# Optimization experiments

Hardware: AMD Instinct MI355X
Metric: run time of the kernel (lower is better)

The kernel has to match this reference:

```python
import jax, jax.numpy as jnp
import numpy as np

IN_CAPS, OUT_CAPS, OUT_DIM = 32, 10, 16


def squash(s):
    # s: [B, out_caps, out_dim]
    sq = jnp.sum(s * s, axis=2)              # [B, out_caps]
    mod = jnp.sqrt(sq)
    scale = sq / (1.0 + sq) / mod            # matches torch: sqrmod/(1+sqrmod)/mod
    return scale[..., None] * s


def setup_inputs() -> dict:
    key = jax.random.key(0)
    k1, k2 = jax.random.split(key)
    B, in_dim = 4096, 288
    caps_output = jax.random.normal(k1, (B, IN_CAPS, in_dim), dtype=jnp.float32)
    # W initialized uniform(-1/32, 1/32) in the original; scale randn similarly small
    W = jax.random.uniform(k2, (IN_CAPS, in_dim, OUT_CAPS * OUT_DIM),
                           dtype=jnp.float32, minval=-1.0 / 32, maxval=1.0 / 32)
    b = jnp.zeros((IN_CAPS, OUT_CAPS), dtype=jnp.float32)
    return {"caps_output": caps_output, "W": W, "b": b}


def reference(caps_output, W, b):
    B = caps_output.shape[0]
    # caps_output.unsqueeze(2).matmul(W): per-input-capsule matmul
    u = jnp.einsum('bni,nio->bno', caps_output, W)          # [B, 32, 160]
    u = u.reshape(B, IN_CAPS, OUT_CAPS, OUT_DIM)            # [B, 32, 10, 16]

    c = jax.nn.softmax(b, axis=1)                           # [32, 10]
    s = jnp.einsum('no,bnod->bod', c, u)                    # [B, 10, 16]
    v = squash(s)

    b_batch = jnp.broadcast_to(b, (B, IN_CAPS, OUT_CAPS))
    for _ in range(3):
        # agreement: <u_predict, v>
        b_batch = b_batch + jnp.einsum('bnod,bod->bno', u, v)
        c = jax.nn.softmax(b_batch, axis=-1)                # [B, 32, 10]
        s = jnp.einsum('bno,bnod->bod', c, u)
        v = squash(s)
    return v
```

## Files before the change

kernel.cpp:

```cpp
#include <hip/hip_runtime.h>
#include <hip/hip_bf16.h>

#define IN_CAPS 32
#define OUT_CAPS 10
#define NOUT 160
#define KDIM 288
#define BATCH 4096
#define KSTEPS 9
#define CTILES 10
#define STR2 162

typedef __bf16 bf16x8 __attribute__((ext_vector_type(8)));
typedef float  f32x4  __attribute__((ext_vector_type(4)));
typedef __attribute__((address_space(1))) void as1_t;
typedef __attribute__((address_space(3))) void as3_t;

__global__ __launch_bounds__(256) void prep_w(const float* __restrict__ W,
                                              __bf16* __restrict__ Wf) {
    int f = blockIdx.x * 256 + threadIdx.x;
    int j    = f & 7;
    int l    = (f >> 3) & 63;
    int rest = f >> 9;
    int c    = rest % CTILES;
    int tnk  = rest / CTILES;
    int ks   = tnk % KSTEPS;
    int n    = tnk / KSTEPS;
    int k    = ks * 32 + (l >> 4) * 8 + j;
    int col  = c * 16 + (l & 15);
    Wf[f] = (__bf16)W[(n * KDIM + k) * NOUT + col];
}

__global__ __launch_bounds__(256) void gemm_u(const float* __restrict__ caps,
                                              const __bf16* __restrict__ Wf,
                                              uint4* __restrict__ up) {
    __shared__ float  As[2][64 * 32];
    __shared__ __bf16 Bs[2][5120];

    const int n    = blockIdx.y;
    const int rb   = blockIdx.x;
    const int w    = threadIdx.x >> 6;
    const int lane = threadIdx.x & 63;
    const int lm   = lane & 15;
    const int lk   = lane >> 4;

    const int sl0 = w * 128 + lane;
    const int sl1 = sl0 + 64;
    const int r0 = sl0 >> 3, r1 = sl1 >> 3;
    const int c0 = (sl0 & 7) ^ (r0 & 7);
    const int c1 = (sl1 & 7) ^ (r1 & 7);
    const float* ga0 = caps + ((size_t)(rb * 64 + r0) * IN_CAPS + n) * KDIM + c0 * 4;
    const float* ga1 = caps + ((size_t)(rb * 64 + r1) * IN_CAPS + n) * KDIM + c1 * 4;

    const __bf16* wb = Wf + (size_t)n * (KSTEPS * 5120);

#define STAGE(ks, buf) do {                                                          \
    __builtin_amdgcn_global_load_lds((const as1_t*)(ga0 + (ks) * 32),                \
                                     (as3_t*)&As[buf][w * 512],        16, 0, 0);    \
    __builtin_amdgcn_global_load_lds((const as1_t*)(ga1 + (ks) * 32),                \
                                     (as3_t*)&As[buf][w * 512 + 256],  16, 0, 0);    \
    __builtin_amdgcn_global_load_lds((const as1_t*)(wb + (size_t)(ks) * 5120 +       \
                                     (w * 2) * 512 + lane * 8),                      \
                                     (as3_t*)&Bs[buf][(w * 2) * 512],  16, 0, 0);    \
    __builtin_amdgcn_global_load_lds((const as1_t*)(wb + (size_t)(ks) * 5120 +       \
                                     (w * 2 + 1) * 512 + lane * 8),                  \
                                     (as3_t*)&Bs[buf][(w * 2 + 1) * 512], 16, 0, 0); \
    if (w < 2)                                                                       \
        __builtin_amdgcn_global_load_lds((const as1_t*)(wb + (size_t)(ks) * 5120 +   \
                                         (8 + w) * 512 + lane * 8),                  \
                                         (as3_t*)&Bs[buf][(8 + w) * 512], 16, 0, 0); \
} while (0)

    f32x4 acc[CTILES];
#pragma unroll
    for (int ct = 0; ct < CTILES; ++ct) acc[ct] = (f32x4){0.f, 0.f, 0.f, 0.f};

    const int rl = w * 16 + lm;
    const int h0 = ((2 * lk)     ^ (lm & 7)) * 4;
    const int h1 = ((2 * lk + 1) ^ (lm & 7)) * 4;

    STAGE(0, 0);
    __syncthreads();

    for (int ks = 0; ks < KSTEPS; ++ks) {
        if (ks + 1 < KSTEPS) STAGE(ks + 1, (ks + 1) & 1);

        const float*  Ac = As[ks & 1];
        const __bf16* Bc = Bs[ks & 1];
        f32x4 x0 = *(const f32x4*)&Ac[rl * 32 + h0];
        f32x4 x1 = *(const f32x4*)&Ac[rl * 32 + h1];
        bf16x8 a;
        a[0] = (__bf16)x0[0]; a[1] = (__bf16)x0[1];
        a[2] = (__bf16)x0[2]; a[3] = (__bf16)x0[3];
        a[4] = (__bf16)x1[0]; a[5] = (__bf16)x1[1];
        a[6] = (__bf16)x1[2]; a[7] = (__bf16)x1[3];

#pragma unroll
        for (int ct = 0; ct < CTILES; ++ct) {
            bf16x8 bfr = *(const bf16x8*)&Bc[ct * 512 + lane * 8];
            acc[ct] = __builtin_amdgcn_mfma_f32_16x16x32_bf16(a, bfr, acc[ct], 0, 0, 0);
        }
        __syncthreads();
    }

    const int rw = rb * 2 + (w >> 1);
    const int mt = w & 1;
    const size_t cbase = ((((size_t)n * 128 + rw) * 2 + mt) * 5) * 64 + lane;
#pragma unroll
    for (int p = 0; p < 5; ++p) {
        bf16x8 pk;
#pragma unroll
        for (int j = 0; j < 8; ++j)
            pk[j] = (__bf16)acc[2 * p + (j >> 2)][j & 3];
        up[cbase + (size_t)p * 64] = __builtin_bit_cast(uint4, pk);
    }
#undef STAGE
}

__global__ __launch_bounds__(256) void routing(const uint4* __restrict__ up,
                                               const float* __restrict__ bbias,
                                               float* __restrict__ out) {
    __shared__ __bf16 ul[4][IN_CAPS * STR2];
    __shared__ float  bl[4][IN_CAPS * OUT_CAPS];
    __shared__ float  cs[4][IN_CAPS * OUT_CAPS];
    __shared__ float  ss[4][NOUT];
    __shared__ float  vs[4][NOUT];
    __shared__ float  scale_s[4][16];

    const int t  = threadIdx.x;
    const int b0 = blockIdx.x * 4;
    const int rw = b0 >> 5;
    const int mt = (b0 >> 4) & 1;
    const int lk = (b0 >> 2) & 3;

    for (int c = t; c < 2560; c += 256) {
        int n   = c / 80;
        int rem = c - n * 80;
        int p   = rem >> 4;
        int lm  = rem & 15;
        size_t idx = ((((size_t)n * 128 + rw) * 2 + mt) * 5 + p) * 64 + lk * 16 + lm;
        bf16x8 v = __builtin_bit_cast(bf16x8, up[idx]);
#pragma unroll
        for (int j = 0; j < 8; ++j) {
            int ct = 2 * p + (j >> 2);
            int rr = j & 3;
            ul[rr][n * STR2 + ct * 16 + lm] = v[j];
        }
    }
    const int grp = t >> 6;
    const int g   = t & 63;
    for (int pp = g; pp < IN_CAPS * OUT_CAPS; pp += 64) bl[grp][pp] = bbias[pp];
    __syncthreads();

    for (int it = 0; it < 4; ++it) {
        if (it > 0) {
            for (int pp = g; pp < IN_CAPS * OUT_CAPS; pp += 64) {
                int n = pp & 31;
                int o = pp >> 5;
                float a = 0.f;
#pragma unroll
                for (int d = 0; d < 16; ++d)
                    a += (float)ul[grp][n * STR2 + o * 16 + d] * vs[grp][o * 16 + d];
                bl[grp][n * 10 + o] += a;
            }
            __syncthreads();
        }
        if (g < IN_CAPS) {
            float m = bl[grp][g * 10];
#pragma unroll
            for (int o = 1; o < 10; ++o) m = fmaxf(m, bl[grp][g * 10 + o]);
            float e[10];
            float sum = 0.f;
#pragma unroll
            for (int o = 0; o < 10; ++o) { e[o] = __expf(bl[grp][g * 10 + o] - m); sum += e[o]; }
            float inv = 1.0f / sum;
#pragma unroll
            for (int o = 0; o < 10; ++o) cs[grp][g * 10 + o] = e[o] * inv;
        }
        __syncthreads();
        for (int p = g; p < NOUT; p += 64) {
            int o = p >> 4;
            float a = 0.f;
#pragma unroll
            for (int nn = 0; nn < IN_CAPS; ++nn)
                a += cs[grp][nn * 10 + o] * (float)ul[grp][nn * STR2 + p];
            ss[grp][p] = a;
        }
        __syncthreads();
        if (g < OUT_CAPS) {
            float sq = 0.f;
#pragma unroll
            for (int d = 0; d < 16; ++d) { float x = ss[grp][g * 16 + d]; sq += x * x; }
            scale_s[grp][g] = sq / ((1.0f + sq) * sqrtf(sq));
        }
        __syncthreads();
        for (int p = g; p < NOUT; p += 64) vs[grp][p] = scale_s[grp][p >> 4] * ss[grp][p];
        __syncthreads();
    }

    for (int p = g; p < NOUT; p += 64)
        out[(size_t)(b0 + grp) * NOUT + p] = vs[grp][p];
}

extern "C" void kernel_launch(void* const* d_in, const int* in_sizes, int n_in,
                              void* d_out, int out_size, void* d_ws, size_t ws_size,
                              hipStream_t stream) {
    const float* caps  = (const float*)d_in[0];
    const float* W     = (const float*)d_in[1];
    const float* bbias = (const float*)d_in[2];
    float* out = (float*)d_out;

    __bf16* Wf = (__bf16*)d_ws;
    uint4*  up = (uint4*)((char*)d_ws + 2949120);

    prep_w<<<dim3(5760), dim3(256), 0, stream>>>(W, Wf);
    gemm_u<<<dim3(64, 32), dim3(256), 0, stream>>>(caps, Wf, up);
    routing<<<dim3(BATCH / 4), dim3(256), 0, stream>>>(up, bbias, out);
}
```

Measured before the change: 78.87 us.

## Deepen GEMM pipeline to four LDS buffers with vmcnt waits

Replaces the double-buffered LDS pipeline in gemm_u with a 4-buffer ring that prefetches three k-steps ahead. Explicit s_waitcnt vmcnt counts plus one s_barrier per step stand in for the two __syncthreads per iteration. The grid is flattened to 1D with n as the fast index, so neighbouring blocks share caps rows. This costs twice the LDS per block, which may lower occupancy. Correctness relies on the hand-computed vmcnt counts and on 4 buffers being enough to avoid write-after-read hazards with a single barrier.

```diff
diff --git a/kernel.cpp b/kernel.cpp
--- a/kernel.cpp
+++ b/kernel.cpp
@@ -30,14 +30,25 @@
     Wf[f] = (__bf16)W[(n * KDIM + k) * NOUT + col];
 }
 
+__device__ __forceinline__ void waitv(int n) {
+    switch (n) {
+        case 0:  asm volatile("s_waitcnt vmcnt(0)"  ::: "memory"); break;
+        case 4:  asm volatile("s_waitcnt vmcnt(4)"  ::: "memory"); break;
+        case 5:  asm volatile("s_waitcnt vmcnt(5)"  ::: "memory"); break;
+        case 8:  asm volatile("s_waitcnt vmcnt(8)"  ::: "memory"); break;
+        default: asm volatile("s_waitcnt vmcnt(10)" ::: "memory"); break;
+    }
+}
+
 __global__ __launch_bounds__(256) void gemm_u(const float* __restrict__ caps,
                                               const __bf16* __restrict__ Wf,
                                               uint4* __restrict__ up) {
-    __shared__ float  As[2][64 * 32];
-    __shared__ __bf16 Bs[2][5120];
-
-    const int n    = blockIdx.y;
-    const int rb   = blockIdx.x;
+    __shared__ float  As[4][64 * 32];
+    __shared__ __bf16 Bs[4][5120];
+
+    const int lin  = blockIdx.x;
+    const int n    = lin & 31;
+    const int rb   = lin >> 5;
     const int w    = threadIdx.x >> 6;
     const int lane = threadIdx.x & 63;
     const int lm   = lane & 15;
@@ -50,24 +61,24 @@
     const int c1 = (sl1 & 7) ^ (r1 & 7);
     const float* ga0 = caps + ((size_t)(rb * 64 + r0) * IN_CAPS + n) * KDIM + c0 * 4;
     const float* ga1 = caps + ((size_t)(rb * 64 + r1) * IN_CAPS + n) * KDIM + c1 * 4;
-
     const __bf16* wb = Wf + (size_t)n * (KSTEPS * 5120);
 
-#define STAGE(ks, buf) do {                                                          \
+#define STAGE(ks) do {                                                               \
+    const int _bf = (ks) & 3;                                                        \
     __builtin_amdgcn_global_load_lds((const as1_t*)(ga0 + (ks) * 32),                \
-                                     (as3_t*)&As[buf][w * 512],        16, 0, 0);    \
+                                     (as3_t*)&As[_bf][w * 512],        16, 0, 0);    \
     __builtin_amdgcn_global_load_lds((const as1_t*)(ga1 + (ks) * 32),                \
-                                     (as3_t*)&As[buf][w * 512 + 256],  16, 0, 0);    \
+                                     (as3_t*)&As[_bf][w * 512 + 256],  16, 0, 0);    \
     __builtin_amdgcn_global_load_lds((const as1_t*)(wb + (size_t)(ks) * 5120 +       \
                                      (w * 2) * 512 + lane * 8),                      \
-                                     (as3_t*)&Bs[buf][(w * 2) * 512],  16, 0, 0);    \
+                                     (as3_t*)&Bs[_bf][(w * 2) * 512],  16, 0, 0);    \
     __builtin_amdgcn_global_load_lds((const as1_t*)(wb + (size_t)(ks) * 5120 +       \
                                      (w * 2 + 1) * 512 + lane * 8),                  \
-                                     (as3_t*)&Bs[buf][(w * 2 + 1) * 512], 16, 0, 0); \
+                                     (as3_t*)&Bs[_bf][(w * 2 + 1) * 512], 16, 0, 0); \
     if (w < 2)                                                                       \
         __builtin_amdgcn_global_load_lds((const as1_t*)(wb + (size_t)(ks) * 5120 +   \
                                          (8 + w) * 512 + lane * 8),                  \
-                                         (as3_t*)&Bs[buf][(8 + w) * 512], 16, 0, 0); \
+                                         (as3_t*)&Bs[_bf][(8 + w) * 512], 16, 0, 0); \
 } while (0)
 
     f32x4 acc[CTILES];
@@ -77,15 +88,20 @@
     const int rl = w * 16 + lm;
     const int h0 = ((2 * lk)     ^ (lm & 7)) * 4;
     const int h1 = ((2 * lk + 1) ^ (lm & 7)) * 4;
-
-    STAGE(0, 0);
-    __syncthreads();
-
+    const int per_stage = (w < 2) ? 5 : 4;
+
+    STAGE(0); STAGE(1); STAGE(2);
+
+#pragma unroll
     for (int ks = 0; ks < KSTEPS; ++ks) {
-        if (ks + 1 < KSTEPS) STAGE(ks + 1, (ks + 1) & 1);
-
-        const float*  Ac = As[ks & 1];
-        const __bf16* Bc = Bs[ks & 1];
+        const int rem = (8 - ks) < 2 ? (8 - ks) : 2;
+        waitv(per_stage * rem);
+        __builtin_amdgcn_s_barrier();
+        asm volatile("" ::: "memory");
+        if (ks + 3 < KSTEPS) STAGE(ks + 3);
+
+        const float*  Ac = As[ks & 3];
+        const __bf16* Bc = Bs[ks & 3];
         f32x4 x0 = *(const f32x4*)&Ac[rl * 32 + h0];
         f32x4 x1 = *(const f32x4*)&Ac[rl * 32 + h1];
         bf16x8 a;
@@ -99,7 +115,6 @@
             bf16x8 bfr = *(const bf16x8*)&Bc[ct * 512 + lane * 8];
             acc[ct] = __builtin_amdgcn_mfma_f32_16x16x32_bf16(a, bfr, acc[ct], 0, 0, 0);
         }
-        __syncthreads();
     }
 
     const int rw = rb * 2 + (w >> 1);
@@ -213,6 +228,6 @@
     uint4*  up = (uint4*)((char*)d_ws + 2949120);
 
     prep_w<<<dim3(5760), dim3(256), 0, stream>>>(W, Wf);
-    gemm_u<<<dim3(64, 32), dim3(256), 0, stream>>>(caps, Wf, up);
+    gemm_u<<<dim3(2048), dim3(256), 0, stream>>>(caps, Wf, up);
     routing<<<dim3(BATCH / 4), dim3(256), 0, stream>>>(up, bbias, out);
 }
```

Measured after the change: 83.64 us. +6.1%, slower.
